# Optimization experiments

Hardware: AMD Instinct MI355X
Metric: run time of the kernel (lower is better)

The kernel has to match this reference:

```python
import jax, jax.numpy as jnp
import numpy as np

B, C, H, W = 8, 256, 64, 64
K = 3                      # kernel size
DG = 4                     # deformable groups
PAD = (K - 1) // 2
K2 = K * K
GN_GROUPS = 32
EPS = 1e-5


def setup_inputs() -> dict:
    key = jax.random.key(0)
    ks = jax.random.split(key, 6)
    x = jax.random.normal(ks[0], (B, C, H, W), dtype=jnp.float32)
    shape = jax.random.normal(ks[1], (B, 4, H, W), dtype=jnp.float32)
    # 1x1 offset conv weight [dg*k*k*2, 4] (bias=False); small std keeps offsets sane
    w_offset = jax.random.normal(ks[2], (DG * K2 * 2, 4), dtype=jnp.float32) * 0.1
    # deformable conv weight [out_c, in_c, K, K]
    w_deform = jax.random.normal(ks[3], (C, C, K, K), dtype=jnp.float32) * 0.01
    gamma = jnp.ones((C,), dtype=jnp.float32)
    beta = jnp.zeros((C,), dtype=jnp.float32)
    return {"x": x, "shape": shape, "w_offset": w_offset,
            "w_deform": w_deform, "gamma": gamma, "beta": beta}


def _bilinear_sample(img, py, px):
    # img: [Cg, H, W]; py, px: [K2, H, W] absolute sampling coords
    h, w = img.shape[1], img.shape[2]
    y0 = jnp.floor(py)
    x0 = jnp.floor(px)
    ly = py - y0
    lx = px - x0

    def gather(yi, xi):
        valid = ((yi >= 0) & (yi <= h - 1) & (xi >= 0) & (xi <= w - 1)).astype(img.dtype)
        yc = jnp.clip(yi, 0, h - 1).astype(jnp.int32)
        xc = jnp.clip(xi, 0, w - 1).astype(jnp.int32)
        return img[:, yc, xc] * valid  # [Cg, K2, H, W]

    v00 = gather(y0, x0)
    v01 = gather(y0, x0 + 1)
    v10 = gather(y0 + 1, x0)
    v11 = gather(y0 + 1, x0 + 1)
    return (v00 * (1 - ly) * (1 - lx) + v01 * (1 - ly) * lx
            + v10 * ly * (1 - lx) + v11 * ly * lx)


def _forward(x, shape, w_offset, w_deform, gamma, beta):
    # offset = 1x1 conv on shape (detached in torch): [B, DG*K2*2, H, W]
    offset = jnp.einsum('oc,bchw->bohw', w_offset, shape)
    # mmcv layout: per group, per kernel position, (dy, dx)
    off = offset.reshape(B, DG, K2, 2, H, W)
    dy, dx = off[:, :, :, 0], off[:, :, :, 1]  # [B, DG, K2, H, W]

    ki = (jnp.arange(K2) // K - PAD).astype(jnp.float32)  # kernel row offsets
    kj = (jnp.arange(K2) % K - PAD).astype(jnp.float32)
    ys = jnp.arange(H, dtype=jnp.float32)
    xs = jnp.arange(W, dtype=jnp.float32)
    # absolute sampling positions [B, DG, K2, H, W]
    py = dy + ki[None, None, :, None, None] + ys[None, None, None, :, None]
    px = dx + kj[None, None, :, None, None] + xs[None, None, None, None, :]

    cg = C // DG
    x_g = x.reshape(B, DG, cg, H, W)
    # sampled: [B, DG, Cg, K2, H, W]
    sampled = jax.vmap(jax.vmap(_bilinear_sample))(x_g, py, px)

    w = w_deform.reshape(C, DG, cg, K2)
    out = jnp.einsum('bgckhw,ogck->bohw', sampled, w)  # [B, C, H, W]

    # GroupNorm(32, C) + ReLU
    og = out.reshape(B, GN_GROUPS, C // GN_GROUPS, H, W)
    mu = og.mean(axis=(2, 3, 4), keepdims=True)
    var = og.var(axis=(2, 3, 4), keepdims=True)
    norm = ((og - mu) * jax.lax.rsqrt(var + EPS)).reshape(B, C, H, W)
    y = norm * gamma[None, :, None, None] + beta[None, :, None, None]
    return jax.nn.relu(y)


def reference(x, shape, w_offset, w_deform, gamma, beta):
    return _forward(x, shape, w_offset, w_deform, gamma, beta)
```

## Files before the change

### kernel.cpp

```cpp
#include <hip/hip_runtime.h>
#include <hip/hip_bf16.h>

#define EPSV 1e-5f

typedef __attribute__((ext_vector_type(8))) short short8;
typedef __attribute__((ext_vector_type(4))) float f32x4;
typedef __attribute__((ext_vector_type(2))) float f32x2;
typedef __attribute__((ext_vector_type(4))) unsigned u32x4;

#define W2_BYTES 1179648ull

__global__ __launch_bounds__(256) void wt2_kernel(const float* __restrict__ wd,
                                                  __hip_bfloat16* __restrict__ w2,
                                                  float* __restrict__ st) {
  int idx = blockIdx.x * 256 + threadIdx.x;
  int c  = idx & 31;
  int r  = idx >> 5;
  int k  = r % 9;
  int r2 = r / 9;
  int p  = r2 & 7;
  int o  = r2 >> 3;
  w2[idx] = __float2bfloat16(wd[(o * 256 + p * 32 + c) * 9 + k]);
  if (blockIdx.x < 2) st[blockIdx.x * 256 + threadIdx.x] = 0.f;
}

static __device__ __forceinline__ f32x2 unpk(unsigned u) {
  union { unsigned i; float f; } lo, hi;
  lo.i = u << 16;
  hi.i = u & 0xffff0000u;
  return (f32x2){lo.f, hi.f};
}

static __device__ __forceinline__ unsigned pkbf(float a, float b) {
  __hip_bfloat162 p = __float22bfloat162_rn(make_float2(a, b));
  return *(unsigned*)&p;
}

__global__ __launch_bounds__(512, 2) void fused_kernel(
    const float* __restrict__ x, const float* __restrict__ shp,
    const float* __restrict__ woff, const __hip_bfloat16* __restrict__ w2,
    float* __restrict__ out, float* __restrict__ st) {
  __shared__ __align__(16) unsigned short sX[2][8 * 64 * 32];
  __shared__ __align__(16) unsigned short sB[2][128 * 64];
  __shared__ float sW[288];

  const int b    = blockIdx.x & 7;
  const int band = blockIdx.x >> 3;
  const int h0   = band << 1;
  const int t    = threadIdx.x;
  const int wv   = t >> 6, lane = t & 63;
  const int quad = lane >> 4, l15 = lane & 15;

  const float* xb = x + ((size_t)b << 20);
  const unsigned short* w2b = (const unsigned short*)w2;

  if (t < 288) sW[t] = woff[t];

  if (wv < 4) {
    const int cw = wv;
    const unsigned short* aro =
        w2b + (size_t)((cw << 6) + l15) * 2304 + (quad << 3);

    f32x4 acc[4][8];
#pragma unroll
    for (int mo = 0; mo < 4; ++mo)
#pragma unroll
      for (int np = 0; np < 8; ++np) acc[mo][np] = (f32x4){0.f, 0.f, 0.f, 0.f};

    short8 afc[2][4];
#pragma unroll
    for (int ks = 0; ks < 2; ++ks)
#pragma unroll
      for (int mo = 0; mo < 4; ++mo)
        afc[ks][mo] = *(const short8*)(aro + (size_t)(mo << 4) * 2304 + (ks << 5));

    asm volatile("s_waitcnt lgkmcnt(0)" ::: "memory");
    asm volatile("s_barrier" ::: "memory");
    asm volatile("s_barrier" ::: "memory");

    for (int it = 0; it < 36; ++it) {
      const unsigned short* Bc = sB[it & 1];
#pragma unroll
      for (int np = 0; np < 8; ++np) {
        const int row = (np << 4) + l15;
#pragma unroll
        for (int ks = 0; ks < 2; ++ks) {
          short8 bf = *(const short8*)&Bc[(row << 6) +
                         ((((ks << 2) + quad) ^ (row & 7)) << 3)];
#pragma unroll
          for (int mo = 0; mo < 4; ++mo)
            acc[mo][np] = __builtin_amdgcn_mfma_f32_16x16x32_bf16(afc[ks][mo], bf, acc[mo][np], 0, 0, 0);
        }
      }
      if (it < 35) {
#pragma unroll
        for (int ks = 0; ks < 2; ++ks)
#pragma unroll
          for (int mo = 0; mo < 4; ++mo)
            afc[ks][mo] = *(const short8*)(aro + (size_t)(mo << 4) * 2304 +
                                           (size_t)((it + 1) << 6) + (ks << 5));
      }
      asm volatile("s_barrier" ::: "memory");
    }

#pragma unroll
    for (int mo = 0; mo < 4; ++mo) {
      float s = 0.f, q = 0.f;
#pragma unroll
      for (int np = 0; np < 8; ++np)
#pragma unroll
        for (int r = 0; r < 4; ++r) { float v = acc[mo][np][r]; s += v; q += v * v; }
#pragma unroll
      for (int m = 1; m < 16; m <<= 1) { s += __shfl_xor(s, m, 64); q += __shfl_xor(q, m, 64); }
      if (l15 == 0) {
        int gid = (b << 5) + (cw << 3) + (mo << 1) + (quad >> 1);
        atomicAdd(&st[gid], s);
        atomicAdd(&st[256 + gid], q);
      }
    }

    float* ob = out + (((size_t)((b << 8) + (cw << 6))) << 12) + (band << 7);
#pragma unroll
    for (int mo = 0; mo < 4; ++mo)
#pragma unroll
      for (int np = 0; np < 8; ++np)
#pragma unroll
        for (int r = 0; r < 4; ++r)
          ob[((size_t)((mo << 4) + (quad << 2) + r) << 12) + (np << 4) + l15] = acc[mo][np][r];
  } else {
    const int pid     = t - 256;
    const int pxn     = pid & 127;
    const int tapslot = pid >> 7;
    const int pxl     = pxn & 63;
    const int h       = h0 + (pxn >> 6);
    const int spx     = pid & 63;
    const int sc8     = (pid >> 6) & 3;
    const int wslot   = (sc8 ^ ((spx >> 1) & 3)) << 3;

    float a0 = shp[((size_t)(b * 4 + 0) << 12) + (h << 6) + pxl];
    float a1 = shp[((size_t)(b * 4 + 1) << 12) + (h << 6) + pxl];
    float a2 = shp[((size_t)(b * 4 + 2) << 12) + (h << 6) + pxl];
    float a3 = shp[((size_t)(b * 4 + 3) << 12) + (h << 6) + pxl];

    {
      const float* xph = xb + ((size_t)(sc8 << 3) << 12) + spx;
#pragma unroll
      for (int j = 0; j < 8; ++j) {
        const int grow = min(max(h0 - 3 + j, 0), 63);
        float v[8];
#pragma unroll
        for (int jj = 0; jj < 8; ++jj) v[jj] = xph[(jj << 12) + (grow << 6)];
        *(u32x4*)&sX[0][((((j << 6) + spx) << 5)) + wslot] =
            (u32x4){pkbf(v[0], v[1]), pkbf(v[2], v[3]), pkbf(v[4], v[5]), pkbf(v[6], v[7])};
      }
    }

    auto produce = [&](int g, int buf) {
      const int ph  = (g * 57) >> 9;
      const int tap = g - ph * 9;
      const int kr  = (tap * 11) >> 5;
      const int kc  = tap - kr * 3;
      const float* wp = &sW[(((ph >> 1) * 9 + tap)) << 3];
      float dy = wp[0]*a0 + wp[1]*a1 + wp[2]*a2 + wp[3]*a3;
      float dx = wp[4]*a0 + wp[5]*a1 + wp[6]*a2 + wp[7]*a3;
      float py  = dy + (float)(h + kr - 1);
      float pxp = dx + (float)(pxl + kc - 1);
      float y0f = floorf(py), x0f = floorf(pxp);
      float ly = py - y0f, lx = pxp - x0f;
      int y0 = (int)y0f, x0 = (int)x0f;
      float m_y0 = (y0 >=  0 && y0 <= 63) ? 1.f : 0.f;
      float m_y1 = (y0 >= -1 && y0 <= 62) ? 1.f : 0.f;
      float m_x0 = (x0 >=  0 && x0 <= 63) ? 1.f : 0.f;
      float m_x1 = (x0 >= -1 && x0 <= 62) ? 1.f : 0.f;
      float w00 = (1.f - ly) * (1.f - lx) * m_y0 * m_x0;
      float w01 = (1.f - ly) * lx         * m_y0 * m_x1;
      float w10 = ly         * (1.f - lx) * m_y1 * m_x0;
      float w11 = ly         * lx         * m_y1 * m_x1;
      int yc0 = min(max(y0, 0), 63),     yc1 = min(max(y0 + 1, 0), 63);
      int xc0 = min(max(x0, 0), 63),     xc1 = min(max(x0 + 1, 0), 63);
      int ry0 = min(max(yc0 - (h0 - 3), 0), 7);
      int ry1 = min(max(yc1 - (h0 - 3), 0), 7);
      const unsigned short* Xc = sX[ph & 1];
      const int z0 = (xc0 >> 1) & 3, z1 = (xc1 >> 1) & 3;
      const int e00 = ((ry0 << 6) + xc0) << 5, e01 = ((ry0 << 6) + xc1) << 5;
      const int e10 = ((ry1 << 6) + xc0) << 5, e11 = ((ry1 << 6) + xc1) << 5;
      uint4 Av[4], Bv[4], Cv[4], Dv[4];
#pragma unroll
      for (int j = 0; j < 4; ++j) {
        Av[j] = *(const uint4*)&Xc[e00 + ((j ^ z0) << 3)];
        Bv[j] = *(const uint4*)&Xc[e01 + ((j ^ z1) << 3)];
        Cv[j] = *(const uint4*)&Xc[e10 + ((j ^ z0) << 3)];
        Dv[j] = *(const uint4*)&Xc[e11 + ((j ^ z1) << 3)];
      }
#pragma unroll
      for (int j = 0; j < 4; ++j) {
        unsigned ua[4] = {Av[j].x, Av[j].y, Av[j].z, Av[j].w};
        unsigned ub[4] = {Bv[j].x, Bv[j].y, Bv[j].z, Bv[j].w};
        unsigned uc[4] = {Cv[j].x, Cv[j].y, Cv[j].z, Cv[j].w};
        unsigned ud[4] = {Dv[j].x, Dv[j].y, Dv[j].z, Dv[j].w};
        unsigned ov[4];
#pragma unroll
        for (int q = 0; q < 4; ++q) {
          f32x2 v = unpk(ua[q]) * w00 + unpk(ub[q]) * w01
                  + unpk(uc[q]) * w10 + unpk(ud[q]) * w11;
          ov[q] = pkbf(v.x, v.y);
        }
        *(u32x4*)&sB[buf][(pxn << 6) + ((((tapslot << 2) + j) ^ (pxn & 7)) << 3)] =
            (u32x4){ov[0], ov[1], ov[2], ov[3]};
      }
    };

    asm volatile("s_waitcnt lgkmcnt(0)" ::: "memory");
    asm volatile("s_barrier" ::: "memory");

    produce(tapslot, 0);
    asm volatile("s_waitcnt lgkmcnt(0)" ::: "memory");
    asm volatile("s_barrier" ::: "memory");

    for (int it = 0; it < 36; ++it) {
      int s = -1, r0 = 0, nr = 0;
      if (it <= 2) { s = 1; r0 = it * 3; nr = (it == 2) ? 2 : 3; }
      else if (it >= 4 && it <= 29) {
        const int u = it - 4;
        const int pair = (u * 57) >> 9;
        const int v = u - pair * 9;
        if (v < 4)      { s = 2 + (pair << 1); r0 = v << 1; nr = 2; }
        else if (v < 8) { s = 3 + (pair << 1); r0 = (v - 4) << 1; nr = 2; }
      }
      float xr[3][8];
      if (s > 0) {
        const float* xph = xb + ((size_t)((s << 5) + (sc8 << 3)) << 12) + spx;
#pragma unroll
        for (int rr = 0; rr < 3; ++rr)
          if (rr < nr) {
            const int grow = min(max(h0 - 3 + r0 + rr, 0), 63);
#pragma unroll
            for (int jj = 0; jj < 8; ++jj) xr[rr][jj] = xph[(jj << 12) + (grow << 6)];
          }
      }
      if (it < 35) produce(((it + 1) << 1) + tapslot, (it + 1) & 1);
      if (s > 0) {
#pragma unroll
        for (int rr = 0; rr < 3; ++rr)
          if (rr < nr) {
            *(u32x4*)&sX[s & 1][((((r0 + rr) << 6) + spx) << 5) + wslot] =
                (u32x4){pkbf(xr[rr][0], xr[rr][1]), pkbf(xr[rr][2], xr[rr][3]),
                        pkbf(xr[rr][4], xr[rr][5]), pkbf(xr[rr][6], xr[rr][7])};
          }
      }
      asm volatile("s_waitcnt lgkmcnt(0)" ::: "memory");
      asm volatile("s_barrier" ::: "memory");
    }
  }
}

__global__ __launch_bounds__(256) void norm_kernel(float* __restrict__ o,
    const float* __restrict__ st, const float* __restrict__ gamma,
    const float* __restrict__ beta) {
  int idx = blockIdx.x * 256 + threadIdx.x;
  f32x4* p = (f32x4*)o;
  int c = (idx >> 10) & 255;
  int b = idx >> 18;
  int g = b * 32 + (c >> 3);
  const float invn = 1.f / 32768.f;
  float mu  = st[g] * invn;
  float var = st[256 + g] * invn - mu * mu;
  float ga = gamma[c] * rsqrtf(var + EPSV);
  float be = beta[c] - mu * ga;
  f32x4 v = p[idx];
  v.x = fmaxf(fmaf(v.x, ga, be), 0.f);
  v.y = fmaxf(fmaf(v.y, ga, be), 0.f);
  v.z = fmaxf(fmaf(v.z, ga, be), 0.f);
  v.w = fmaxf(fmaf(v.w, ga, be), 0.f);
  __builtin_nontemporal_store(v, &p[idx]);
}

extern "C" void kernel_launch(void* const* d_in, const int* in_sizes, int n_in,
                              void* d_out, int out_size, void* d_ws, size_t ws_size,
                              hipStream_t stream) {
  const float* x     = (const float*)d_in[0];
  const float* shp   = (const float*)d_in[1];
  const float* woff  = (const float*)d_in[2];
  const float* wdef  = (const float*)d_in[3];
  const float* gamma = (const float*)d_in[4];
  const float* beta  = (const float*)d_in[5];
  float* out = (float*)d_out;
  __hip_bfloat16* w2 = (__hip_bfloat16*)d_ws;
  float* st          = (float*)((char*)d_ws + W2_BYTES);

  hipLaunchKernelGGL(wt2_kernel,   dim3(2304), dim3(256), 0, stream, wdef, w2, st);
  hipLaunchKernelGGL(fused_kernel, dim3(256),  dim3(512), 0, stream, x, shp, woff, w2, out, st);
  hipLaunchKernelGGL(norm_kernel,  dim3(8192), dim3(256), 0, stream, out, st, gamma, beta);
}
```

Baseline: 179.5 us.

## Replace block barriers with LDS flag handshakes and quad-buffered producer/consumer ring

Swaps the lockstep s_barrier between the MFMA consumer waves and the bilinear-sampling producer waves for per-slot LDS counters, and grows the sampled-tile buffer from 2 to 4 slots so producers can run ahead of consumers. Producers only rendezvous among themselves when an input-channel staging slice is reloaded, and they get raised scheduling priority. The goal is to hide the skew between the two roles. The cost is more LDS, spin-wait polling on volatile shared ints, and a risk of subtle ordering bugs.

```diff
diff --git a/kernel.cpp b/kernel.cpp
--- a/kernel.cpp
+++ b/kernel.cpp
@@ -41,8 +41,9 @@
     const float* __restrict__ woff, const __hip_bfloat16* __restrict__ w2,
     float* __restrict__ out, float* __restrict__ st) {
   __shared__ __align__(16) unsigned short sX[2][8 * 64 * 32];
-  __shared__ __align__(16) unsigned short sB[2][128 * 64];
+  __shared__ __align__(16) unsigned short sB[4][128 * 64];
   __shared__ float sW[288];
+  __shared__ int flg[9];
 
   const int b    = blockIdx.x & 7;
   const int band = blockIdx.x >> 3;
@@ -54,7 +55,8 @@
   const float* xb = x + ((size_t)b << 20);
   const unsigned short* w2b = (const unsigned short*)w2;
 
-  if (t < 288) sW[t] = woff[t];
+  if (t < 9) flg[t] = 0;
+  __syncthreads();
 
   if (wv < 4) {
     const int cw = wv;
@@ -74,12 +76,15 @@
       for (int mo = 0; mo < 4; ++mo)
         afc[ks][mo] = *(const short8*)(aro + (size_t)(mo << 4) * 2304 + (ks << 5));
 
-    asm volatile("s_waitcnt lgkmcnt(0)" ::: "memory");
-    asm volatile("s_barrier" ::: "memory");
-    asm volatile("s_barrier" ::: "memory");
-
-    for (int it = 0; it < 36; ++it) {
-      const unsigned short* Bc = sB[it & 1];
+    for (int j = 0; j < 36; ++j) {
+      {
+        const int need = ((j >> 2) + 1) << 2;
+        volatile int* fr = (volatile int*)&flg[j & 3];
+        while (*fr < need) {}
+      }
+      asm volatile("" ::: "memory");
+      __builtin_amdgcn_sched_barrier(0);
+      const unsigned short* Bc = sB[j & 3];
 #pragma unroll
       for (int np = 0; np < 8; ++np) {
         const int row = (np << 4) + l15;
@@ -92,15 +97,16 @@
             acc[mo][np] = __builtin_amdgcn_mfma_f32_16x16x32_bf16(afc[ks][mo], bf, acc[mo][np], 0, 0, 0);
         }
       }
-      if (it < 35) {
+      if (j < 35) {
 #pragma unroll
         for (int ks = 0; ks < 2; ++ks)
 #pragma unroll
           for (int mo = 0; mo < 4; ++mo)
             afc[ks][mo] = *(const short8*)(aro + (size_t)(mo << 4) * 2304 +
-                                           (size_t)((it + 1) << 6) + (ks << 5));
-      }
-      asm volatile("s_barrier" ::: "memory");
+                                           (size_t)((j + 1) << 6) + (ks << 5));
+      }
+      asm volatile("s_waitcnt lgkmcnt(0)" ::: "memory");
+      if (lane == 0) atomicAdd(&flg[4 + (j & 3)], 1);
     }
 
 #pragma unroll
@@ -128,6 +134,7 @@
         for (int r = 0; r < 4; ++r)
           ob[((size_t)((mo << 4) + (quad << 2) + r) << 12) + (np << 4) + l15] = acc[mo][np][r];
   } else {
+    __builtin_amdgcn_s_setprio(1);
     const int pid     = t - 256;
     const int pxn     = pid & 127;
     const int tapslot = pid >> 7;
@@ -137,6 +144,8 @@
     const int sc8     = (pid >> 6) & 3;
     const int wslot   = (sc8 ^ ((spx >> 1) & 3)) << 3;
 
+    for (int i = pid; i < 288; i += 256) sW[i] = woff[i];
+
     float a0 = shp[((size_t)(b * 4 + 0) << 12) + (h << 6) + pxl];
     float a1 = shp[((size_t)(b * 4 + 1) << 12) + (h << 6) + pxl];
     float a2 = shp[((size_t)(b * 4 + 2) << 12) + (h << 6) + pxl];
@@ -154,13 +163,17 @@
             (u32x4){pkbf(v[0], v[1]), pkbf(v[2], v[3]), pkbf(v[4], v[5]), pkbf(v[6], v[7])};
       }
     }
-
-    auto produce = [&](int g, int buf) {
-      const int ph  = (g * 57) >> 9;
-      const int tap = g - ph * 9;
-      const int kr  = (tap * 11) >> 5;
-      const int kc  = tap - kr * 3;
-      const float* wp = &sW[(((ph >> 1) * 9 + tap)) << 3];
+    asm volatile("s_waitcnt lgkmcnt(0)" ::: "memory");
+    if (lane == 0) atomicAdd(&flg[8], 1);
+    { volatile int* fp = (volatile int*)&flg[8]; while (*fp < 4) {} }
+    asm volatile("" ::: "memory");
+    __builtin_amdgcn_sched_barrier(0);
+
+    auto produce = [&](int tap, int slot) {
+      const int ph = tap / 9;
+      const int tk = tap - ph * 9;
+      const int kr = tk / 3, kc = tk - kr * 3;
+      const float* wp = &sW[(((ph >> 1) * 9 + tk)) << 3];
       float dy = wp[0]*a0 + wp[1]*a1 + wp[2]*a2 + wp[3]*a3;
       float dx = wp[4]*a0 + wp[5]*a1 + wp[6]*a2 + wp[7]*a3;
       float py  = dy + (float)(h + kr - 1);
@@ -205,51 +218,57 @@
                   + unpk(uc[q]) * w10 + unpk(ud[q]) * w11;
           ov[q] = pkbf(v.x, v.y);
         }
-        *(u32x4*)&sB[buf][(pxn << 6) + ((((tapslot << 2) + j) ^ (pxn & 7)) << 3)] =
+        *(u32x4*)&sB[slot][(pxn << 6) + ((((tapslot << 2) + j) ^ (pxn & 7)) << 3)] =
             (u32x4){ov[0], ov[1], ov[2], ov[3]};
       }
     };
 
-    asm volatile("s_waitcnt lgkmcnt(0)" ::: "memory");
-    asm volatile("s_barrier" ::: "memory");
-
-    produce(tapslot, 0);
-    asm volatile("s_waitcnt lgkmcnt(0)" ::: "memory");
-    asm volatile("s_barrier" ::: "memory");
-
-    for (int it = 0; it < 36; ++it) {
-      int s = -1, r0 = 0, nr = 0;
-      if (it <= 2) { s = 1; r0 = it * 3; nr = (it == 2) ? 2 : 3; }
-      else if (it >= 4 && it <= 29) {
-        const int u = it - 4;
-        const int pair = (u * 57) >> 9;
-        const int v = u - pair * 9;
-        if (v < 4)      { s = 2 + (pair << 1); r0 = v << 1; nr = 2; }
-        else if (v < 8) { s = 3 + (pair << 1); r0 = (v - 4) << 1; nr = 2; }
-      }
-      float xr[3][8];
-      if (s > 0) {
+    int rdvK = 1;
+    for (int j = 0; j < 36; ++j) {
+      if (j == 4 || j == 5 || j == 9 || j == 13 || j == 14 ||
+          j == 18 || j == 22 || j == 23 || j == 27 || j == 31) {
+        asm volatile("s_waitcnt lgkmcnt(0)" ::: "memory");
+        if (lane == 0) atomicAdd(&flg[8], 1);
+        ++rdvK;
+        const int needR = rdvK << 2;
+        volatile int* fp = (volatile int*)&flg[8];
+        while (*fp < needR) {}
+        asm volatile("" ::: "memory");
+        __builtin_amdgcn_sched_barrier(0);
+      }
+      int s = 0, m = 0;
+      if (j <= 3)                  { s = 1;                  m = j; }
+      else if (j >= 5 && j <= 12)  { s = 2 + ((j - 5) >> 2);  m = (j - 5) & 3; }
+      else if (j >= 14 && j <= 21) { s = 4 + ((j - 14) >> 2); m = (j - 14) & 3; }
+      else if (j >= 23 && j <= 30) { s = 6 + ((j - 23) >> 2); m = (j - 23) & 3; }
+      float xrA[8], xrB[8];
+      if (s) {
         const float* xph = xb + ((size_t)((s << 5) + (sc8 << 3)) << 12) + spx;
-#pragma unroll
-        for (int rr = 0; rr < 3; ++rr)
-          if (rr < nr) {
-            const int grow = min(max(h0 - 3 + r0 + rr, 0), 63);
-#pragma unroll
-            for (int jj = 0; jj < 8; ++jj) xr[rr][jj] = xph[(jj << 12) + (grow << 6)];
-          }
-      }
-      if (it < 35) produce(((it + 1) << 1) + tapslot, (it + 1) & 1);
-      if (s > 0) {
-#pragma unroll
-        for (int rr = 0; rr < 3; ++rr)
-          if (rr < nr) {
-            *(u32x4*)&sX[s & 1][((((r0 + rr) << 6) + spx) << 5) + wslot] =
-                (u32x4){pkbf(xr[rr][0], xr[rr][1]), pkbf(xr[rr][2], xr[rr][3]),
-                        pkbf(xr[rr][4], xr[rr][5]), pkbf(xr[rr][6], xr[rr][7])};
-          }
+        const int g0 = min(max(h0 - 3 + (m << 1), 0), 63);
+        const int g1 = min(max(h0 - 2 + (m << 1), 0), 63);
+#pragma unroll
+        for (int jj = 0; jj < 8; ++jj) xrA[jj] = xph[(jj << 12) + (g0 << 6)];
+#pragma unroll
+        for (int jj = 0; jj < 8; ++jj) xrB[jj] = xph[(jj << 12) + (g1 << 6)];
+      }
+      {
+        const int need = (j >> 2) << 2;
+        volatile int* fd = (volatile int*)&flg[4 + (j & 3)];
+        while (*fd < need) {}
+      }
+      asm volatile("" ::: "memory");
+      __builtin_amdgcn_sched_barrier(0);
+      produce((j << 1) + tapslot, j & 3);
+      if (s) {
+        *(u32x4*)&sX[s & 1][((((m << 1) << 6) + spx) << 5) + wslot] =
+            (u32x4){pkbf(xrA[0], xrA[1]), pkbf(xrA[2], xrA[3]),
+                    pkbf(xrA[4], xrA[5]), pkbf(xrA[6], xrA[7])};
+        *(u32x4*)&sX[s & 1][(((((m << 1) + 1) << 6) + spx) << 5) + wslot] =
+            (u32x4){pkbf(xrB[0], xrB[1]), pkbf(xrB[2], xrB[3]),
+                    pkbf(xrB[4], xrB[5]), pkbf(xrB[6], xrB[7])};
       }
       asm volatile("s_waitcnt lgkmcnt(0)" ::: "memory");
-      asm volatile("s_barrier" ::: "memory");
+      if (lane == 0) atomicAdd(&flg[j & 3], 1);
     }
   }
 }
```

After: 183.9 us. 1.02x slower.

## Fuse GroupNorm+ReLU into main kernel via grid-wide atomic barrier

Applied to the files above, without the earlier changes.

Drops the separate normalization kernel. After accumulating the per-group sum and sum of squares, every block waits on a global atomic counter until all 256 blocks have contributed. It then applies the GroupNorm affine transform and ReLU directly from registers before writing the output. This removes a full extra read and write of the output tensor and one kernel launch. The cost is a spin-wait barrier that assumes all blocks are co-resident, and output stores can no longer overlap other blocks' compute. The weight transform kernel also now reads the source weights in coalesced order and scatters the writes instead.

```diff
diff --git a/kernel.cpp b/kernel.cpp
--- a/kernel.cpp
+++ b/kernel.cpp
@@ -14,14 +14,15 @@
                                                   __hip_bfloat16* __restrict__ w2,
                                                   float* __restrict__ st) {
   int idx = blockIdx.x * 256 + threadIdx.x;
-  int c  = idx & 31;
-  int r  = idx >> 5;
-  int k  = r % 9;
-  int r2 = r / 9;
-  int p  = r2 & 7;
-  int o  = r2 >> 3;
-  w2[idx] = __float2bfloat16(wd[(o * 256 + p * 32 + c) * 9 + k]);
-  if (blockIdx.x < 2) st[blockIdx.x * 256 + threadIdx.x] = 0.f;
+  float v = wd[idx];
+  int o   = idx / 2304;
+  int rem = idx - o * 2304;
+  int cin = rem / 9;
+  int k   = rem - cin * 9;
+  int p   = cin >> 5;
+  int c   = cin & 31;
+  w2[o * 2304 + p * 288 + k * 32 + c] = __float2bfloat16(v);
+  if (idx < 576) st[idx] = 0.f;
 }
 
 static __device__ __forceinline__ f32x2 unpk(unsigned u) {
@@ -39,6 +40,7 @@
 __global__ __launch_bounds__(512, 2) void fused_kernel(
     const float* __restrict__ x, const float* __restrict__ shp,
     const float* __restrict__ woff, const __hip_bfloat16* __restrict__ w2,
+    const float* __restrict__ gamma, const float* __restrict__ beta,
     float* __restrict__ out, float* __restrict__ st) {
   __shared__ __align__(16) unsigned short sX[2][8 * 64 * 32];
   __shared__ __align__(16) unsigned short sB[2][128 * 64];
@@ -53,6 +55,7 @@
 
   const float* xb = x + ((size_t)b << 20);
   const unsigned short* w2b = (const unsigned short*)w2;
+  int* cnt = (int*)(st + 512);
 
   if (t < 288) sW[t] = woff[t];
 
@@ -119,14 +122,37 @@
       }
     }
 
+    __threadfence();
+    __syncthreads();
+    if (t == 0) {
+      __hip_atomic_fetch_add(cnt, 1, __ATOMIC_ACQ_REL, __HIP_MEMORY_SCOPE_AGENT);
+      while (__hip_atomic_load(cnt, __ATOMIC_ACQUIRE, __HIP_MEMORY_SCOPE_AGENT) < 256) {}
+    }
+    __syncthreads();
+
+    const float invn = 1.f / 32768.f;
     float* ob = out + (((size_t)((b << 8) + (cw << 6))) << 12) + (band << 7);
 #pragma unroll
-    for (int mo = 0; mo < 4; ++mo)
-#pragma unroll
-      for (int np = 0; np < 8; ++np)
-#pragma unroll
-        for (int r = 0; r < 4; ++r)
-          ob[((size_t)((mo << 4) + (quad << 2) + r) << 12) + (np << 4) + l15] = acc[mo][np][r];
+    for (int mo = 0; mo < 4; ++mo) {
+      const int gid = (b << 5) + (cw << 3) + (mo << 1) + (quad >> 1);
+      float sS = __hip_atomic_load(&st[gid],       __ATOMIC_RELAXED, __HIP_MEMORY_SCOPE_AGENT);
+      float sQ = __hip_atomic_load(&st[256 + gid], __ATOMIC_RELAXED, __HIP_MEMORY_SCOPE_AGENT);
+      float mu  = sS * invn;
+      float var = sQ * invn - mu * mu;
+      float rs  = rsqrtf(var + EPSV);
+#pragma unroll
+      for (int r = 0; r < 4; ++r) {
+        const int och = (cw << 6) + (mo << 4) + (quad << 2) + r;
+        float ga = gamma[och] * rs;
+        float be = beta[och] - mu * ga;
+        float* orow = ob + ((size_t)((mo << 4) + (quad << 2) + r) << 12);
+#pragma unroll
+        for (int np = 0; np < 8; ++np) {
+          float v = fmaxf(fmaf(acc[mo][np][r], ga, be), 0.f);
+          __builtin_nontemporal_store(v, &orow[(np << 4) + l15]);
+        }
+      }
+    }
   } else {
     const int pid     = t - 256;
     const int pxn     = pid & 127;
@@ -251,28 +277,11 @@
       asm volatile("s_waitcnt lgkmcnt(0)" ::: "memory");
       asm volatile("s_barrier" ::: "memory");
     }
+
+    __threadfence();
+    __syncthreads();
+    __syncthreads();
   }
-}
-
-__global__ __launch_bounds__(256) void norm_kernel(float* __restrict__ o,
-    const float* __restrict__ st, const float* __restrict__ gamma,
-    const float* __restrict__ beta) {
-  int idx = blockIdx.x * 256 + threadIdx.x;
-  f32x4* p = (f32x4*)o;
-  int c = (idx >> 10) & 255;
-  int b = idx >> 18;
-  int g = b * 32 + (c >> 3);
-  const float invn = 1.f / 32768.f;
-  float mu  = st[g] * invn;
-  float var = st[256 + g] * invn - mu * mu;
-  float ga = gamma[c] * rsqrtf(var + EPSV);
-  float be = beta[c] - mu * ga;
-  f32x4 v = p[idx];
-  v.x = fmaxf(fmaf(v.x, ga, be), 0.f);
-  v.y = fmaxf(fmaf(v.y, ga, be), 0.f);
-  v.z = fmaxf(fmaf(v.z, ga, be), 0.f);
-  v.w = fmaxf(fmaf(v.w, ga, be), 0.f);
-  __builtin_nontemporal_store(v, &p[idx]);
 }
 
 extern "C" void kernel_launch(void* const* d_in, const int* in_sizes, int n_in,
@@ -289,6 +298,6 @@
   float* st          = (float*)((char*)d_ws + W2_BYTES);
 
   hipLaunchKernelGGL(wt2_kernel,   dim3(2304), dim3(256), 0, stream, wdef, w2, st);
-  hipLaunchKernelGGL(fused_kernel, dim3(256),  dim3(512), 0, stream, x, shp, woff, w2, out, st);
-  hipLaunchKernelGGL(norm_kernel,  dim3(8192), dim3(256), 0, stream, out, st, gamma, beta);
-}
+  hipLaunchKernelGGL(fused_kernel, dim3(256),  dim3(512), 0, stream,
+                     x, shp, woff, w2, gamma, beta, out, st);
+}
```

New measurement: 211.0 us. +17.6%, slower.
